# Kernel optimization log

Measured on AMD Instinct MI355X. Metric: run time of the kernel, lower is better.

The kernel has to match this reference:

```python
import jax, jax.numpy as jnp
import numpy as np

N_NODES = 100000
N_EDGES = 1200000
D_FEAT = 64


def setup_inputs() -> dict:
    key = jax.random.key(0)
    k1, k2, k3 = jax.random.split(key, 3)
    feat = jax.random.normal(k1, (N_NODES, D_FEAT), dtype=jnp.float32)
    eps = jnp.zeros((1,), dtype=jnp.float32)
    edge_src = jax.random.randint(k2, (N_EDGES,), 0, N_NODES, dtype=jnp.int32)
    edge_dst = jax.random.randint(k3, (N_EDGES,), 0, N_NODES, dtype=jnp.int32)
    return {"feat": feat, "eps": eps, "edge_src": edge_src, "edge_dst": edge_dst}


def reference(feat, eps, edge_src, edge_dst):
    # DGL update_all(copy_u('h','m'), sum('m','neigh')):
    # gather source-node features along edges, segment-sum into destination nodes.
    messages = feat[edge_src]  # [E, D] gather
    neigh = jax.ops.segment_sum(messages, edge_dst, num_segments=N_NODES)  # [N, D]
    # eps-scaled residual: (1 + eps) * feat + neigh
    return (1.0 + eps) * feat + neigh
```

## Files before the change

kernel.cpp:

```cpp
#include <hip/hip_runtime.h>


#define N_NODES 100000
#define D_FEAT  64
#define N_EDGES 1200000

#define BSHIFT  6
#define NPB     64
#define KB      ((N_NODES + NPB - 1) / NPB)
#define CAP_B   1024
#define NCAP    32
#define OVL_CAP 128
#define CNT_STRIDE 16

#define PB       128
#define PTH      1024
#define EPB      ((N_EDGES + PB - 1) / PB)
#define BN       10
#define CAST_ITEMS (N_NODES * D_FEAT / 8)
#define CAST_BLOCKS ((CAST_ITEMS + PTH - 1) / PTH)

__device__ __forceinline__ unsigned short f32_to_bf16_rne(float f) {
    unsigned int u = __float_as_uint(f);
    u += 0x7fffu + ((u >> 16) & 1u);
    return (unsigned short)(u >> 16);
}
__device__ __forceinline__ float bf_lo(unsigned int q) { return __uint_as_float(q << 16); }
__device__ __forceinline__ float bf_hi(unsigned int q) { return __uint_as_float(q & 0xffff0000u); }

__global__ __launch_bounds__(1024) void gin_cast_place_kernel(
    const float* __restrict__ feat,
    const int* __restrict__ edge_src,
    const int* __restrict__ edge_dst,
    unsigned int* __restrict__ fb,
    int* __restrict__ bcnt,
    int* __restrict__ buckets)
{
    const int tid = threadIdx.x;
    if (blockIdx.x < PB) {
        __shared__ int hist[KB];
        __shared__ int base[KB];
        __shared__ int lcur[KB];
        for (int k = tid; k < KB; k += PTH) { hist[k] = 0; lcur[k] = 0; }
        __syncthreads();

        const int e0 = blockIdx.x * EPB;
        const int e1 = min(e0 + EPB, N_EDGES);

        int d[BN], s[BN]; bool v[BN];
        #pragma unroll
        for (int u = 0; u < BN; ++u) {
            const int ee = e0 + tid + u * PTH;
            v[u] = (ee < e1);
            if (v[u]) { d[u] = edge_dst[ee]; s[u] = edge_src[ee]; }
        }
        #pragma unroll
        for (int u = 0; u < BN; ++u)
            if (v[u]) atomicAdd(&hist[d[u] >> BSHIFT], 1);
        __syncthreads();

        for (int k = tid; k < KB; k += PTH) {
            const int h = hist[k];
            if (h > 0) base[k] = atomicAdd(&bcnt[k * CNT_STRIDE], h);
        }
        __syncthreads();

        int t[BN];
        #pragma unroll
        for (int u = 0; u < BN; ++u)
            if (v[u]) t[u] = base[d[u] >> BSHIFT] + atomicAdd(&lcur[d[u] >> BSHIFT], 1);
        #pragma unroll
        for (int u = 0; u < BN; ++u) {
            if (v[u]) {
                const int k = d[u] >> BSHIFT;
                if (t[u] < CAP_B)
                    buckets[k * CAP_B + t[u]] = s[u] | ((d[u] & (NPB - 1)) << 17);
            }
        }
    } else {
        const int i = (blockIdx.x - PB) * PTH + tid;
        if (i < CAST_ITEMS) {
            const float4 f0 = reinterpret_cast<const float4*>(feat)[2 * i];
            const float4 f1 = reinterpret_cast<const float4*>(feat)[2 * i + 1];
            uint4 q;
            q.x = (unsigned)f32_to_bf16_rne(f0.x) | ((unsigned)f32_to_bf16_rne(f0.y) << 16);
            q.y = (unsigned)f32_to_bf16_rne(f0.z) | ((unsigned)f32_to_bf16_rne(f0.w) << 16);
            q.z = (unsigned)f32_to_bf16_rne(f1.x) | ((unsigned)f32_to_bf16_rne(f1.y) << 16);
            q.w = (unsigned)f32_to_bf16_rne(f1.z) | ((unsigned)f32_to_bf16_rne(f1.w) << 16);
            reinterpret_cast<uint4*>(fb)[i] = q;
        }
    }
}

__global__ __launch_bounds__(256) void gin_gather_kernel(
    const float* __restrict__ feat,
    const unsigned int* __restrict__ fb,
    const float* __restrict__ eps,
    const int* __restrict__ bcnt,
    const int* __restrict__ buckets,
    float* __restrict__ out)
{
    __shared__ int lcnt[NPB];
    __shared__ int sl[NPB * NCAP];
    __shared__ int2 ovl[OVL_CAP];
    __shared__ int ovl_n;
    const int tid  = threadIdx.x;
    const int k    = blockIdx.x;
    const int lane = tid & 63;
    const int w    = tid >> 6;

    if (tid < NPB) lcnt[tid] = 0;
    if (tid == 0) ovl_n = 0;
    __syncthreads();

    int m = bcnt[k * CNT_STRIDE];
    if (m > CAP_B) m = CAP_B;
    const int* __restrict__ bkt = buckets + k * CAP_B;
    for (int i = tid; i < m; i += 256) {
        const int e  = bkt[i];
        const int ld = e >> 17;
        const int t  = atomicAdd(&lcnt[ld], 1);
        if (t < NCAP) sl[ld * NCAP + t] = e & 0x1FFFF;
        else {
            const int o = atomicAdd(&ovl_n, 1);
            if (o < OVL_CAP) ovl[o] = make_int2(e & 0x1FFFF, ld);
        }
    }
    __syncthreads();

    const int r = lane >> 4;
    const int c = lane & 15;
    const float scale = 1.0f + eps[0];
    const int node_base = k * NPB;

    for (int nl = w * 16; nl < w * 16 + 16; nl += 4) {
        const int node0 = node_base + nl;
        int n0 = lcnt[nl];     if (n0 > NCAP) n0 = NCAP;
        int n1 = lcnt[nl + 1]; if (n1 > NCAP) n1 = NCAP;
        int n2 = lcnt[nl + 2]; if (n2 > NCAP) n2 = NCAP;
        int n3 = lcnt[nl + 3]; if (n3 > NCAP) n3 = NCAP;
        const int ll = lane & (NCAP - 1);
        const int my0 = sl[(nl)     * NCAP + ll];
        const int my1 = sl[(nl + 1) * NCAP + ll];
        const int my2 = sl[(nl + 2) * NCAP + ll];
        const int my3 = sl[(nl + 3) * NCAP + ll];

        float a0 = 0.f, a1 = 0.f, a2 = 0.f, a3 = 0.f;
        float b0 = 0.f, b1 = 0.f, b2 = 0.f, b3 = 0.f;
        float c0 = 0.f, c1 = 0.f, c2 = 0.f, c3 = 0.f;
        float d0 = 0.f, d1 = 0.f, d2 = 0.f, d3 = 0.f;
        int nmax = n0;
        if (n1 > nmax) nmax = n1;
        if (n2 > nmax) nmax = n2;
        if (n3 > nmax) nmax = n3;
        for (int j0 = 0; j0 < nmax; j0 += 4) {
            const int j  = j0 + r;
            const int j0c = (j < n0) ? j : 0;
            const int j1c = (j < n1) ? j : 0;
            const int j2c = (j < n2) ? j : 0;
            const int j3c = (j < n3) ? j : 0;
            const int s0 = __shfl(my0, j0c);
            const int s1 = __shfl(my1, j1c);
            const int s2 = __shfl(my2, j2c);
            const int s3 = __shfl(my3, j3c);
            if (j < n0) {
                const uint2 q = *reinterpret_cast<const uint2*>(&fb[s0 * (D_FEAT / 2) + c * 2]);
                a0 += bf_lo(q.x); a1 += bf_hi(q.x);
                a2 += bf_lo(q.y); a3 += bf_hi(q.y);
            }
            if (j < n1) {
                const uint2 q = *reinterpret_cast<const uint2*>(&fb[s1 * (D_FEAT / 2) + c * 2]);
                b0 += bf_lo(q.x); b1 += bf_hi(q.x);
                b2 += bf_lo(q.y); b3 += bf_hi(q.y);
            }
            if (j < n2) {
                const uint2 q = *reinterpret_cast<const uint2*>(&fb[s2 * (D_FEAT / 2) + c * 2]);
                c0 += bf_lo(q.x); c1 += bf_hi(q.x);
                c2 += bf_lo(q.y); c3 += bf_hi(q.y);
            }
            if (j < n3) {
                const uint2 q = *reinterpret_cast<const uint2*>(&fb[s3 * (D_FEAT / 2) + c * 2]);
                d0 += bf_lo(q.x); d1 += bf_hi(q.x);
                d2 += bf_lo(q.y); d3 += bf_hi(q.y);
            }
        }
        a0 += __shfl_xor(a0, 16); a1 += __shfl_xor(a1, 16);
        a2 += __shfl_xor(a2, 16); a3 += __shfl_xor(a3, 16);
        b0 += __shfl_xor(b0, 16); b1 += __shfl_xor(b1, 16);
        b2 += __shfl_xor(b2, 16); b3 += __shfl_xor(b3, 16);
        c0 += __shfl_xor(c0, 16); c1 += __shfl_xor(c1, 16);
        c2 += __shfl_xor(c2, 16); c3 += __shfl_xor(c3, 16);
        d0 += __shfl_xor(d0, 16); d1 += __shfl_xor(d1, 16);
        d2 += __shfl_xor(d2, 16); d3 += __shfl_xor(d3, 16);
        a0 += __shfl_xor(a0, 32); a1 += __shfl_xor(a1, 32);
        a2 += __shfl_xor(a2, 32); a3 += __shfl_xor(a3, 32);
        b0 += __shfl_xor(b0, 32); b1 += __shfl_xor(b1, 32);
        b2 += __shfl_xor(b2, 32); b3 += __shfl_xor(b3, 32);
        c0 += __shfl_xor(c0, 32); c1 += __shfl_xor(c1, 32);
        c2 += __shfl_xor(c2, 32); c3 += __shfl_xor(c3, 32);
        d0 += __shfl_xor(d0, 32); d1 += __shfl_xor(d1, 32);
        d2 += __shfl_xor(d2, 32); d3 += __shfl_xor(d3, 32);

        if (r == 0) {
            #pragma unroll
            for (int q4 = 0; q4 < 4; ++q4) {
                const int node = node0 + q4;
                if (node < N_NODES) {
                    float s0v, s1v, s2v, s3v;
                    if (q4 == 0) { s0v = a0; s1v = a1; s2v = a2; s3v = a3; }
                    else if (q4 == 1) { s0v = b0; s1v = b1; s2v = b2; s3v = b3; }
                    else if (q4 == 2) { s0v = c0; s1v = c1; s2v = c2; s3v = c3; }
                    else { s0v = d0; s1v = d1; s2v = d2; s3v = d3; }
                    const float4 f = *reinterpret_cast<const float4*>(&feat[node * D_FEAT + c * 4]);
                    float4 o;
                    o.x = scale * f.x + s0v; o.y = scale * f.y + s1v;
                    o.z = scale * f.z + s2v; o.w = scale * f.w + s3v;
                    *reinterpret_cast<float4*>(&out[node * D_FEAT + c * 4]) = o;
                }
            }
        }
    }

    __syncthreads();
    int on = ovl_n; if (on > OVL_CAP) on = OVL_CAP;
    for (int i = w; i < on; i += 4) {
        const int2 ov = ovl[i];
        atomicAdd(&out[(node_base + ov.y) * D_FEAT + lane],
                  feat[ov.x * D_FEAT + lane]);
    }
}

__global__ __launch_bounds__(256) void gin_init_kernel(
    const float* __restrict__ feat, const float* __restrict__ eps, float* __restrict__ out)
{
    const float scale = 1.0f + eps[0];
    int i = blockIdx.x * blockDim.x + threadIdx.x;
    if (i < (N_NODES * D_FEAT) / 4) {
        float4 v = reinterpret_cast<const float4*>(feat)[i];
        v.x *= scale; v.y *= scale; v.z *= scale; v.w *= scale;
        reinterpret_cast<float4*>(out)[i] = v;
    }
}
__global__ __launch_bounds__(256) void gin_scatter_kernel(
    const float* __restrict__ feat, const int* __restrict__ edge_src,
    const int* __restrict__ edge_dst, float* __restrict__ out)
{
    const int edge = blockIdx.x * 4 + (threadIdx.x >> 6);
    const int lane = threadIdx.x & 63;
    if (edge < N_EDGES)
        atomicAdd(&out[edge_dst[edge] * D_FEAT + lane], feat[edge_src[edge] * D_FEAT + lane]);
}

extern "C" void kernel_launch(void* const* d_in, const int* in_sizes, int n_in,
                              void* d_out, int out_size, void* d_ws, size_t ws_size,
                              hipStream_t stream)
{
    const float* feat     = (const float*)d_in[0];
    const float* eps      = (const float*)d_in[1];
    const int*   edge_src = (const int*)d_in[2];
    const int*   edge_dst = (const int*)d_in[3];
    float* out = (float*)d_out;

    const size_t fb_ints   = (size_t)N_NODES * D_FEAT / 2;
    const size_t bcnt_ints = (size_t)KB * CNT_STRIDE;
    const size_t bkt_ints  = (size_t)KB * CAP_B;
    const size_t need = sizeof(int) * (fb_ints + bcnt_ints + bkt_ints);
    if (ws_size >= need) {
        unsigned int* fb = (unsigned int*)d_ws;
        int* bcnt    = (int*)(fb + fb_ints);
        int* buckets = bcnt + bcnt_ints;

        hipMemsetAsync(bcnt, 0, bcnt_ints * sizeof(int), stream);

        gin_cast_place_kernel<<<PB + CAST_BLOCKS, PTH, 0, stream>>>(
            feat, edge_src, edge_dst, fb, bcnt, buckets);
        gin_gather_kernel<<<KB, 256, 0, stream>>>(
            feat, fb, eps, bcnt, buckets, out);
    } else {
        const int total4 = (N_NODES * D_FEAT) / 4;
        gin_init_kernel<<<(total4 + 255) / 256, 256, 0, stream>>>(feat, eps, out);
        gin_scatter_kernel<<<(N_EDGES + 3) / 4, 256, 0, stream>>>(
            feat, edge_src, edge_dst, out);
    }
}
```

Before: 139.6 us.

## Fuse memset, cast/place and gather into one cooperative grid-synced kernel

Replaces the memset plus two-kernel sequence with a single cooperative kernel of 512 blocks of 1024 threads. The kernel zeroes the bucket counters, runs the histogram alongside the bf16 cast, then after a grid sync does the bucket placement, and after a second grid sync does the per-bucket gather. Each block handles four buckets in the gather phase using separate shared-memory slices. This removes launch gaps and the separate memset, at the cost of two grid-wide barriers, a second read of edge_dst, and higher per-block LDS use. The old path stays as a fallback when cooperative launch or occupancy is insufficient.

New measurement: 140.6 us. About the same (+0.7%).

```diff
diff --git a/kernel.cpp b/kernel.cpp
--- a/kernel.cpp
+++ b/kernel.cpp
@@ -1,4 +1,5 @@
 #include <hip/hip_runtime.h>
+#include <hip/hip_cooperative_groups.h>
 
 
 #define N_NODES 100000
@@ -15,11 +16,15 @@
 
 #define PB       128
 #define PTH      1024
+#define GB       512
+#define CB       (GB - PB)
 #define EPB      ((N_EDGES + PB - 1) / PB)
 #define BN       10
 #define CAST_ITEMS (N_NODES * D_FEAT / 8)
 #define CAST_BLOCKS ((CAST_ITEMS + PTH - 1) / PTH)
 
+namespace cg = cooperative_groups;
+
 __device__ __forceinline__ unsigned short f32_to_bf16_rne(float f) {
     unsigned int u = __float_as_uint(f);
     u += 0x7fffu + ((u >> 16) & 1u);
@@ -28,102 +33,120 @@
 __device__ __forceinline__ float bf_lo(unsigned int q) { return __uint_as_float(q << 16); }
 __device__ __forceinline__ float bf_hi(unsigned int q) { return __uint_as_float(q & 0xffff0000u); }
 
-__global__ __launch_bounds__(1024) void gin_cast_place_kernel(
+__device__ __forceinline__ uint4 cast_pack(const float* __restrict__ feat, int i) {
+    const float4 f0 = reinterpret_cast<const float4*>(feat)[2 * i];
+    const float4 f1 = reinterpret_cast<const float4*>(feat)[2 * i + 1];
+    uint4 q;
+    q.x = (unsigned)f32_to_bf16_rne(f0.x) | ((unsigned)f32_to_bf16_rne(f0.y) << 16);
+    q.y = (unsigned)f32_to_bf16_rne(f0.z) | ((unsigned)f32_to_bf16_rne(f0.w) << 16);
+    q.z = (unsigned)f32_to_bf16_rne(f1.x) | ((unsigned)f32_to_bf16_rne(f1.y) << 16);
+    q.w = (unsigned)f32_to_bf16_rne(f1.z) | ((unsigned)f32_to_bf16_rne(f1.w) << 16);
+    return q;
+}
+
+__global__ __launch_bounds__(1024, 8) void gin_fused_kernel(
     const float* __restrict__ feat,
+    const float* __restrict__ eps,
     const int* __restrict__ edge_src,
     const int* __restrict__ edge_dst,
     unsigned int* __restrict__ fb,
     int* __restrict__ bcnt,
-    int* __restrict__ buckets)
+    int* __restrict__ buckets,
+    float* __restrict__ out)
 {
+    __shared__ int hist[KB];
+    __shared__ int base[KB];
+    __shared__ int lcur[KB];
+    __shared__ int lcnt4[4][NPB];
+    __shared__ int sl4[4][NPB * NCAP];
+    __shared__ int2 ovl4[4][OVL_CAP];
+    __shared__ int ovln4[4];
+
     const int tid = threadIdx.x;
-    if (blockIdx.x < PB) {
-        __shared__ int hist[KB];
-        __shared__ int base[KB];
-        __shared__ int lcur[KB];
+    const int b   = blockIdx.x;
+    cg::grid_group grid = cg::this_grid();
+
+    { const int gt = b * PTH + tid;
+      if (gt < KB * CNT_STRIDE) bcnt[gt] = 0; }
+
+    if (b < PB) {
         for (int k = tid; k < KB; k += PTH) { hist[k] = 0; lcur[k] = 0; }
         __syncthreads();
-
-        const int e0 = blockIdx.x * EPB;
+        const int e0 = b * EPB;
         const int e1 = min(e0 + EPB, N_EDGES);
-
-        int d[BN], s[BN]; bool v[BN];
-        #pragma unroll
-        for (int u = 0; u < BN; ++u) {
-            const int ee = e0 + tid + u * PTH;
-            v[u] = (ee < e1);
-            if (v[u]) { d[u] = edge_dst[ee]; s[u] = edge_src[ee]; }
-        }
-        #pragma unroll
-        for (int u = 0; u < BN; ++u)
-            if (v[u]) atomicAdd(&hist[d[u] >> BSHIFT], 1);
-        __syncthreads();
-
+        for (int e = e0 + tid; e < e1; e += PTH * 8) {
+            int dd[8]; bool vv[8];
+            #pragma unroll
+            for (int u = 0; u < 8; ++u) {
+                const int ee = e + u * PTH;
+                vv[u] = (ee < e1);
+                if (vv[u]) dd[u] = edge_dst[ee];
+            }
+            #pragma unroll
+            for (int u = 0; u < 8; ++u)
+                if (vv[u]) atomicAdd(&hist[dd[u] >> BSHIFT], 1);
+        }
+    } else {
+        for (int i = (b - PB) * PTH + tid; i < CAST_ITEMS; i += CB * PTH)
+            reinterpret_cast<uint4*>(fb)[i] = cast_pack(feat, i);
+    }
+    grid.sync();
+
+    if (b < PB) {
         for (int k = tid; k < KB; k += PTH) {
             const int h = hist[k];
             if (h > 0) base[k] = atomicAdd(&bcnt[k * CNT_STRIDE], h);
         }
         __syncthreads();
-
-        int t[BN];
-        #pragma unroll
-        for (int u = 0; u < BN; ++u)
-            if (v[u]) t[u] = base[d[u] >> BSHIFT] + atomicAdd(&lcur[d[u] >> BSHIFT], 1);
-        #pragma unroll
-        for (int u = 0; u < BN; ++u) {
-            if (v[u]) {
-                const int k = d[u] >> BSHIFT;
-                if (t[u] < CAP_B)
-                    buckets[k * CAP_B + t[u]] = s[u] | ((d[u] & (NPB - 1)) << 17);
-            }
-        }
-    } else {
-        const int i = (blockIdx.x - PB) * PTH + tid;
-        if (i < CAST_ITEMS) {
-            const float4 f0 = reinterpret_cast<const float4*>(feat)[2 * i];
-            const float4 f1 = reinterpret_cast<const float4*>(feat)[2 * i + 1];
-            uint4 q;
-            q.x = (unsigned)f32_to_bf16_rne(f0.x) | ((unsigned)f32_to_bf16_rne(f0.y) << 16);
-            q.y = (unsigned)f32_to_bf16_rne(f0.z) | ((unsigned)f32_to_bf16_rne(f0.w) << 16);
-            q.z = (unsigned)f32_to_bf16_rne(f1.x) | ((unsigned)f32_to_bf16_rne(f1.y) << 16);
-            q.w = (unsigned)f32_to_bf16_rne(f1.z) | ((unsigned)f32_to_bf16_rne(f1.w) << 16);
-            reinterpret_cast<uint4*>(fb)[i] = q;
-        }
-    }
-}
-
-__global__ __launch_bounds__(256) void gin_gather_kernel(
-    const float* __restrict__ feat,
-    const unsigned int* __restrict__ fb,
-    const float* __restrict__ eps,
-    const int* __restrict__ bcnt,
-    const int* __restrict__ buckets,
-    float* __restrict__ out)
-{
-    __shared__ int lcnt[NPB];
-    __shared__ int sl[NPB * NCAP];
-    __shared__ int2 ovl[OVL_CAP];
-    __shared__ int ovl_n;
-    const int tid  = threadIdx.x;
-    const int k    = blockIdx.x;
+        const int e0 = b * EPB;
+        const int e1 = min(e0 + EPB, N_EDGES);
+        for (int e = e0 + tid; e < e1; e += PTH * 8) {
+            int dd[8], ss[8], tt[8]; bool vv[8];
+            #pragma unroll
+            for (int u = 0; u < 8; ++u) {
+                const int ee = e + u * PTH;
+                vv[u] = (ee < e1);
+                if (vv[u]) { dd[u] = edge_dst[ee]; ss[u] = edge_src[ee]; }
+            }
+            #pragma unroll
+            for (int u = 0; u < 8; ++u)
+                if (vv[u]) tt[u] = base[dd[u] >> BSHIFT] + atomicAdd(&lcur[dd[u] >> BSHIFT], 1);
+            #pragma unroll
+            for (int u = 0; u < 8; ++u) {
+                if (vv[u]) {
+                    const int k = dd[u] >> BSHIFT;
+                    if (tt[u] < CAP_B)
+                        buckets[k * CAP_B + tt[u]] = ss[u] | ((dd[u] & (NPB - 1)) << 17);
+                }
+            }
+        }
+    }
+    grid.sync();
+
+    const int g    = tid >> 8;
+    const int t256 = tid & 255;
     const int lane = tid & 63;
-    const int w    = tid >> 6;
-
-    if (tid < NPB) lcnt[tid] = 0;
-    if (tid == 0) ovl_n = 0;
+    const int w2   = (tid >> 6) & 3;
+    const int k    = g * GB + b;
+
+    int* lcnt = lcnt4[g];
+    int* sl   = sl4[g];
+
+    if (t256 < NPB) lcnt[t256] = 0;
+    if (t256 == 0) ovln4[g] = 0;
     __syncthreads();
 
-    int m = bcnt[k * CNT_STRIDE];
-    if (m > CAP_B) m = CAP_B;
-    const int* __restrict__ bkt = buckets + k * CAP_B;
-    for (int i = tid; i < m; i += 256) {
+    int m = 0;
+    if (k < KB) { m = bcnt[k * CNT_STRIDE]; if (m > CAP_B) m = CAP_B; }
+    const int* __restrict__ bkt = buckets + (size_t)k * CAP_B;
+    for (int i = t256; i < m; i += 256) {
         const int e  = bkt[i];
         const int ld = e >> 17;
         const int t  = atomicAdd(&lcnt[ld], 1);
         if (t < NCAP) sl[ld * NCAP + t] = e & 0x1FFFF;
         else {
-            const int o = atomicAdd(&ovl_n, 1);
-            if (o < OVL_CAP) ovl[o] = make_int2(e & 0x1FFFF, ld);
+            const int o = atomicAdd(&ovln4[g], 1);
+            if (o < OVL_CAP) ovl4[g][o] = make_int2(e & 0x1FFFF, ld);
         }
     }
     __syncthreads();
@@ -133,7 +156,7 @@
     const float scale = 1.0f + eps[0];
     const int node_base = k * NPB;
 
-    for (int nl = w * 16; nl < w * 16 + 16; nl += 4) {
+    for (int nl = w2 * 16; nl < w2 * 16 + 16; nl += 4) {
         const int node0 = node_base + nl;
         int n0 = lcnt[nl];     if (n0 > NCAP) n0 = NCAP;
         int n1 = lcnt[nl + 1]; if (n1 > NCAP) n1 = NCAP;
@@ -222,6 +245,197 @@
     }
 
     __syncthreads();
+    int on = ovln4[g]; if (on > OVL_CAP) on = OVL_CAP;
+    for (int i = w2; i < on; i += 4) {
+        const int2 ov = ovl4[g][i];
+        atomicAdd(&out[(node_base + ov.y) * D_FEAT + lane],
+                  feat[ov.x * D_FEAT + lane]);
+    }
+}
+
+__global__ __launch_bounds__(1024) void gin_cast_place_kernel(
+    const float* __restrict__ feat,
+    const int* __restrict__ edge_src,
+    const int* __restrict__ edge_dst,
+    unsigned int* __restrict__ fb,
+    int* __restrict__ bcnt,
+    int* __restrict__ buckets)
+{
+    const int tid = threadIdx.x;
+    if (blockIdx.x < PB) {
+        __shared__ int hist[KB];
+        __shared__ int base[KB];
+        __shared__ int lcur[KB];
+        for (int k = tid; k < KB; k += PTH) { hist[k] = 0; lcur[k] = 0; }
+        __syncthreads();
+
+        const int e0 = blockIdx.x * EPB;
+        const int e1 = min(e0 + EPB, N_EDGES);
+        int d[BN], s[BN]; bool v[BN];
+        #pragma unroll
+        for (int u = 0; u < BN; ++u) {
+            const int ee = e0 + tid + u * PTH;
+            v[u] = (ee < e1);
+            if (v[u]) { d[u] = edge_dst[ee]; s[u] = edge_src[ee]; }
+        }
+        #pragma unroll
+        for (int u = 0; u < BN; ++u)
+            if (v[u]) atomicAdd(&hist[d[u] >> BSHIFT], 1);
+        __syncthreads();
+        for (int k = tid; k < KB; k += PTH) {
+            const int h = hist[k];
+            if (h > 0) base[k] = atomicAdd(&bcnt[k * CNT_STRIDE], h);
+        }
+        __syncthreads();
+        int t[BN];
+        #pragma unroll
+        for (int u = 0; u < BN; ++u)
+            if (v[u]) t[u] = base[d[u] >> BSHIFT] + atomicAdd(&lcur[d[u] >> BSHIFT], 1);
+        #pragma unroll
+        for (int u = 0; u < BN; ++u) {
+            if (v[u]) {
+                const int k = d[u] >> BSHIFT;
+                if (t[u] < CAP_B)
+                    buckets[k * CAP_B + t[u]] = s[u] | ((d[u] & (NPB - 1)) << 17);
+            }
+        }
+    } else {
+        const int i = (blockIdx.x - PB) * PTH + tid;
+        if (i < CAST_ITEMS)
+            reinterpret_cast<uint4*>(fb)[i] = cast_pack(feat, i);
+    }
+}
+
+__global__ __launch_bounds__(256) void gin_gather_kernel(
+    const float* __restrict__ feat,
+    const unsigned int* __restrict__ fb,
+    const float* __restrict__ eps,
+    const int* __restrict__ bcnt,
+    const int* __restrict__ buckets,
+    float* __restrict__ out)
+{
+    __shared__ int lcnt[NPB];
+    __shared__ int sl[NPB * NCAP];
+    __shared__ int2 ovl[OVL_CAP];
+    __shared__ int ovl_n;
+    const int tid  = threadIdx.x;
+    const int k    = blockIdx.x;
+    const int lane = tid & 63;
+    const int w    = tid >> 6;
+
+    if (tid < NPB) lcnt[tid] = 0;
+    if (tid == 0) ovl_n = 0;
+    __syncthreads();
+
+    int m = bcnt[k * CNT_STRIDE];
+    if (m > CAP_B) m = CAP_B;
+    const int* __restrict__ bkt = buckets + k * CAP_B;
+    for (int i = tid; i < m; i += 256) {
+        const int e  = bkt[i];
+        const int ld = e >> 17;
+        const int t  = atomicAdd(&lcnt[ld], 1);
+        if (t < NCAP) sl[ld * NCAP + t] = e & 0x1FFFF;
+        else {
+            const int o = atomicAdd(&ovl_n, 1);
+            if (o < OVL_CAP) ovl[o] = make_int2(e & 0x1FFFF, ld);
+        }
+    }
+    __syncthreads();
+
+    const int r = lane >> 4;
+    const int c = lane & 15;
+    const float scale = 1.0f + eps[0];
+    const int node_base = k * NPB;
+
+    for (int nl = w * 16; nl < w * 16 + 16; nl += 4) {
+        const int node0 = node_base + nl;
+        int n0 = lcnt[nl];     if (n0 > NCAP) n0 = NCAP;
+        int n1 = lcnt[nl + 1]; if (n1 > NCAP) n1 = NCAP;
+        int n2 = lcnt[nl + 2]; if (n2 > NCAP) n2 = NCAP;
+        int n3 = lcnt[nl + 3]; if (n3 > NCAP) n3 = NCAP;
+        const int ll = lane & (NCAP - 1);
+        const int my0 = sl[(nl)     * NCAP + ll];
+        const int my1 = sl[(nl + 1) * NCAP + ll];
+        const int my2 = sl[(nl + 2) * NCAP + ll];
+        const int my3 = sl[(nl + 3) * NCAP + ll];
+
+        float a0 = 0.f, a1 = 0.f, a2 = 0.f, a3 = 0.f;
+        float b0 = 0.f, b1 = 0.f, b2 = 0.f, b3 = 0.f;
+        float c0 = 0.f, c1 = 0.f, c2 = 0.f, c3 = 0.f;
+        float d0 = 0.f, d1 = 0.f, d2 = 0.f, d3 = 0.f;
+        int nmax = n0;
+        if (n1 > nmax) nmax = n1;
+        if (n2 > nmax) nmax = n2;
+        if (n3 > nmax) nmax = n3;
+        for (int j0 = 0; j0 < nmax; j0 += 4) {
+            const int j  = j0 + r;
+            const int j0c = (j < n0) ? j : 0;
+            const int j1c = (j < n1) ? j : 0;
+            const int j2c = (j < n2) ? j : 0;
+            const int j3c = (j < n3) ? j : 0;
+            const int s0 = __shfl(my0, j0c);
+            const int s1 = __shfl(my1, j1c);
+            const int s2 = __shfl(my2, j2c);
+            const int s3 = __shfl(my3, j3c);
+            if (j < n0) {
+                const uint2 q = *reinterpret_cast<const uint2*>(&fb[s0 * (D_FEAT / 2) + c * 2]);
+                a0 += bf_lo(q.x); a1 += bf_hi(q.x);
+                a2 += bf_lo(q.y); a3 += bf_hi(q.y);
+            }
+            if (j < n1) {
+                const uint2 q = *reinterpret_cast<const uint2*>(&fb[s1 * (D_FEAT / 2) + c * 2]);
+                b0 += bf_lo(q.x); b1 += bf_hi(q.x);
+                b2 += bf_lo(q.y); b3 += bf_hi(q.y);
+            }
+            if (j < n2) {
+                const uint2 q = *reinterpret_cast<const uint2*>(&fb[s2 * (D_FEAT / 2) + c * 2]);
+                c0 += bf_lo(q.x); c1 += bf_hi(q.x);
+                c2 += bf_lo(q.y); c3 += bf_hi(q.y);
+            }
+            if (j < n3) {
+                const uint2 q = *reinterpret_cast<const uint2*>(&fb[s3 * (D_FEAT / 2) + c * 2]);
+                d0 += bf_lo(q.x); d1 += bf_hi(q.x);
+                d2 += bf_lo(q.y); d3 += bf_hi(q.y);
+            }
+        }
+        a0 += __shfl_xor(a0, 16); a1 += __shfl_xor(a1, 16);
+        a2 += __shfl_xor(a2, 16); a3 += __shfl_xor(a3, 16);
+        b0 += __shfl_xor(b0, 16); b1 += __shfl_xor(b1, 16);
+        b2 += __shfl_xor(b2, 16); b3 += __shfl_xor(b3, 16);
+        c0 += __shfl_xor(c0, 16); c1 += __shfl_xor(c1, 16);
+        c2 += __shfl_xor(c2, 16); c3 += __shfl_xor(c3, 16);
+        d0 += __shfl_xor(d0, 16); d1 += __shfl_xor(d1, 16);
+        d2 += __shfl_xor(d2, 16); d3 += __shfl_xor(d3, 16);
+        a0 += __shfl_xor(a0, 32); a1 += __shfl_xor(a1, 32);
+        a2 += __shfl_xor(a2, 32); a3 += __shfl_xor(a3, 32);
+        b0 += __shfl_xor(b0, 32); b1 += __shfl_xor(b1, 32);
+        b2 += __shfl_xor(b2, 32); b3 += __shfl_xor(b3, 32);
+        c0 += __shfl_xor(c0, 32); c1 += __shfl_xor(c1, 32);
+        c2 += __shfl_xor(c2, 32); c3 += __shfl_xor(c3, 32);
+        d0 += __shfl_xor(d0, 32); d1 += __shfl_xor(d1, 32);
+        d2 += __shfl_xor(d2, 32); d3 += __shfl_xor(d3, 32);
+
+        if (r == 0) {
+            #pragma unroll
+            for (int q4 = 0; q4 < 4; ++q4) {
+                const int node = node0 + q4;
+                if (node < N_NODES) {
+                    float s0v, s1v, s2v, s3v;
+                    if (q4 == 0) { s0v = a0; s1v = a1; s2v = a2; s3v = a3; }
+                    else if (q4 == 1) { s0v = b0; s1v = b1; s2v = b2; s3v = b3; }
+                    else if (q4 == 2) { s0v = c0; s1v = c1; s2v = c2; s3v = c3; }
+                    else { s0v = d0; s1v = d1; s2v = d2; s3v = d3; }
+                    const float4 f = *reinterpret_cast<const float4*>(&feat[node * D_FEAT + c * 4]);
+                    float4 o;
+                    o.x = scale * f.x + s0v; o.y = scale * f.y + s1v;
+                    o.z = scale * f.z + s2v; o.w = scale * f.w + s3v;
+                    *reinterpret_cast<float4*>(&out[node * D_FEAT + c * 4]) = o;
+                }
+            }
+        }
+    }
+
+    __syncthreads();
     int on = ovl_n; if (on > OVL_CAP) on = OVL_CAP;
     for (int i = w; i < on; i += 4) {
         const int2 ov = ovl[i];
@@ -270,8 +484,31 @@
         int* bcnt    = (int*)(fb + fb_ints);
         int* buckets = bcnt + bcnt_ints;
 
+        static int coop_ok = -1;
+        if (coop_ok < 0) {
+            coop_ok = 0;
+            int dev = 0;
+            if (hipGetDevice(&dev) == hipSuccess) {
+                int attr = 0, ncu = 0, maxb = 0;
+                if (hipDeviceGetAttribute(&attr, hipDeviceAttributeCooperativeLaunch, dev) == hipSuccess &&
+                    attr != 0 &&
+                    hipDeviceGetAttribute(&ncu, hipDeviceAttributeMultiprocessorCount, dev) == hipSuccess &&
+                    hipOccupancyMaxActiveBlocksPerMultiprocessor(&maxb, gin_fused_kernel, PTH, 0) == hipSuccess &&
+                    maxb * ncu >= GB)
+                    coop_ok = 1;
+            }
+        }
+
+        if (coop_ok == 1) {
+            void* kargs[] = { (void*)&feat, (void*)&eps, (void*)&edge_src, (void*)&edge_dst,
+                              (void*)&fb, (void*)&bcnt, (void*)&buckets, (void*)&out };
+            hipError_t err = hipLaunchCooperativeKernel(gin_fused_kernel,
+                                dim3(GB), dim3(PTH), kargs, 0, stream);
+            if (err == hipSuccess) return;
+            coop_ok = 0;
+        }
+
         hipMemsetAsync(bcnt, 0, bcnt_ints * sizeof(int), stream);
-
         gin_cast_place_kernel<<<PB + CAST_BLOCKS, PTH, 0, stream>>>(
             feat, edge_src, edge_dst, fb, bcnt, buckets);
         gin_gather_kernel<<<KB, 256, 0, stream>>>(
```
